# Optimization experiments

Measured on AMD Instinct MI355X. Metric: run time of the kernel, lower is better.

## Reference

```python
import jax, jax.numpy as jnp
import numpy as np

N_NODES = 2048   # active nodes fed to the GCN (= sum(state_flag==1))
N_EDGES = 4096
L = 4096         # obs_dim: padded node count after flag==0 insertions
NHID = 16
GCN_OUT = 16
H1 = 1024
DIN = L * (3 + GCN_OUT)  # 77824


def setup_inputs() -> dict:
    key = jax.random.key(0)
    ks = jax.random.split(key, 14)
    X = jax.random.normal(ks[0], (N_NODES, 1), dtype=jnp.float32)
    Z = jax.random.normal(ks[1], (N_EDGES, 1), dtype=jnp.float32)
    adj_e = jax.random.uniform(ks[2], (N_EDGES, N_EDGES), dtype=jnp.float32) / N_EDGES
    adj_v = jax.random.uniform(ks[3], (N_NODES, N_NODES), dtype=jnp.float32) / N_NODES
    T = jax.random.uniform(ks[4], (N_NODES, N_EDGES), dtype=jnp.float32) / N_EDGES
    state_cost = jax.random.normal(ks[5], (L,), dtype=jnp.float32)
    # exactly N_NODES ones -> static shapes for the vectorized insertion
    state_flag = (jnp.arange(L) % 2).astype(jnp.float32)
    state_dual = jax.random.uniform(ks[6], (N_NODES, 1), dtype=jnp.float32)
    # GCN params (CensNet-style node/edge GCN, eval mode -> no dropout)
    W1 = jax.random.normal(ks[7], (2, NHID), dtype=jnp.float32) * (1.0 / np.sqrt(2.0))
    b1 = jnp.zeros((NHID,), dtype=jnp.float32)
    W2 = jax.random.normal(ks[8], (NHID, GCN_OUT), dtype=jnp.float32) * (1.0 / np.sqrt(NHID))
    b2 = jnp.zeros((GCN_OUT,), dtype=jnp.float32)
    # v_net MLP params
    Wm1 = jax.random.normal(ks[9], (DIN, H1), dtype=jnp.float32) * (1.0 / np.sqrt(DIN))
    bm1 = jnp.zeros((H1,), dtype=jnp.float32)
    Wm2 = jax.random.normal(ks[10], (H1, H1), dtype=jnp.float32) * (1.0 / np.sqrt(H1))
    bm2 = jnp.zeros((H1,), dtype=jnp.float32)
    Wm3 = jax.random.normal(ks[11], (H1, 1), dtype=jnp.float32) * (1.0 / np.sqrt(H1))
    bm3 = jnp.zeros((1,), dtype=jnp.float32)
    return {"X": X, "Z": Z, "adj_e": adj_e, "adj_v": adj_v, "T": T,
            "state_cost": state_cost, "state_flag": state_flag, "state_dual": state_dual,
            "W1": W1, "b1": b1, "W2": W2, "b2": b2,
            "Wm1": Wm1, "bm1": bm1, "Wm2": Wm2, "bm2": bm2, "Wm3": Wm3, "bm3": bm3}


def reference(X, Z, adj_e, adj_v, T, state_cost, state_flag, state_dual,
              W1, b1, W2, b2, Wm1, bm1, Wm2, bm2, Wm3, bm3):
    # --- GCN(nfeat_v=1, nfeat_e=1) -> [N, GCN_OUT] node embeddings ---
    Ze = adj_e @ Z                                 # [E,1] edge convolution
    H0 = jnp.concatenate([X, T @ Ze], axis=1)      # [N,2] node feats + incidence-pooled edge feats
    Hh = jax.nn.relu(adj_v @ (H0 @ W1) + b1)       # [N, NHID]
    emb = adj_v @ (Hh @ W2) + b2                   # [N, GCN_OUT]

    # --- vectorized equivalent of the O(L^2) insertion loop ---
    # row i of the padded embedding is emb[rank_of_i_among_flag==1] if flag[i]==1 else 0
    flag_i = state_flag.astype(jnp.int32)
    src = jnp.clip(jnp.cumsum(flag_i) - 1, 0, emb.shape[0] - 1)   # [L]
    m = state_flag[:, None] > 0                                   # [L,1]
    emb_pad = jnp.where(m, emb[src], 0.0)                         # [L, GCN_OUT]
    dual_pad = jnp.where(m, state_dual[src], 1.0)                 # [L, 1]

    obs = jnp.concatenate([
        jax.nn.log_softmax(state_cost[:, None], axis=0),
        state_flag[:, None],
        dual_pad,
        emb_pad,
    ], axis=1).reshape(-1)                                        # [L*(3+GCN_OUT)]

    # --- v_net MLP: tanh, tanh, identity ---
    h = jnp.tanh(obs @ Wm1 + bm1)
    h = jnp.tanh(h @ Wm2 + bm2)
    v = h @ Wm3 + bm3                                             # [1]
    return jnp.squeeze(v, -1)                                     # scalar
```

## Files before the change

### kernel.cpp

```cpp
#include <hip/hip_runtime.h>
#include <math.h>

#define N_NODES 2048
#define N_EDGES 4096
#define L_DIM   4096
#define H1      1024
#define DIN     (L_DIM * 19)
#define NCHUNK1 1024
#define ROWS1   76
#define NCHUNK2 256
#define ROWS2   4

typedef float v4f __attribute__((ext_vector_type(4)));
__device__ __forceinline__ float4 ntload4(const float4* p) {
    v4f v = __builtin_nontemporal_load((const v4f*)p);
    float4 r; r.x = v.x; r.y = v.y; r.z = v.z; r.w = v.w;
    return r;
}

__global__ void gemv_rows(const float* __restrict__ A, const float* __restrict__ x,
                          float* __restrict__ y, int C4 ) {
    const int tid = threadIdx.x;
    const int row = blockIdx.x;
    const float4* A4 = (const float4*)A + (size_t)row * C4;
    const float4* X4 = (const float4*)x;
    float acc = 0.f;
    #pragma unroll 4
    for (int p = tid; p < C4; p += 256) {
        float4 a = ntload4(A4 + p);
        float4 b = X4[p];
        acc += a.x * b.x + a.y * b.y + a.z * b.z + a.w * b.w;
    }
    acc += __shfl_xor(acc, 1);  acc += __shfl_xor(acc, 2);  acc += __shfl_xor(acc, 4);
    acc += __shfl_xor(acc, 8);  acc += __shfl_xor(acc, 16); acc += __shfl_xor(acc, 32);
    __shared__ float s[4];
    if ((tid & 63) == 0) s[tid >> 6] = acc;
    __syncthreads();
    if (tid == 0) y[row] = s[0] + s[1] + s[2] + s[3];
}

__global__ void gemv_T_p1(const float* __restrict__ T, const float* __restrict__ Ze,
                          const float* __restrict__ X, const float* __restrict__ W1,
                          float* __restrict__ P1) {
    const int tid = threadIdx.x;
    const int row = blockIdx.x;
    const float4* A4 = (const float4*)T + (size_t)row * (N_EDGES / 4);
    const float4* X4 = (const float4*)Ze;
    float acc = 0.f;
    #pragma unroll 4
    for (int p = tid; p < N_EDGES / 4; p += 256) {
        float4 a = ntload4(A4 + p);
        float4 b = X4[p];
        acc += a.x * b.x + a.y * b.y + a.z * b.z + a.w * b.w;
    }
    acc += __shfl_xor(acc, 1);  acc += __shfl_xor(acc, 2);  acc += __shfl_xor(acc, 4);
    acc += __shfl_xor(acc, 8);  acc += __shfl_xor(acc, 16); acc += __shfl_xor(acc, 32);
    __shared__ float s[4];
    if ((tid & 63) == 0) s[tid >> 6] = acc;
    __syncthreads();
    if (tid < 16) {
        const float tze = s[0] + s[1] + s[2] + s[3];
        P1[(row >> 2) * 64 + tid * 4 + (row & 3)] = X[row] * W1[tid] + tze * W1[16 + tid];
    }
}

__global__ __launch_bounds__(256) void adjmul_lds(
        const float* __restrict__ A, const float* __restrict__ P,
        const float* __restrict__ bias, const float* __restrict__ W2,
        float* __restrict__ outp, int fuse_p2) {
    __shared__ float As[8][2052];
    __shared__ float hs[8][16];
    const int tid = threadIdx.x;
    const int row0 = blockIdx.x * 8;
    const float4* Ag = (const float4*)A;
    #pragma unroll
    for (int r = 0; r < 8; ++r) {
        float4 v0 = ntload4(Ag + (size_t)(row0 + r) * 512 + tid);
        float4 v1 = ntload4(Ag + (size_t)(row0 + r) * 512 + 256 + tid);
        *(float4*)&As[r][tid * 4] = v0;
        *(float4*)&As[r][1024 + tid * 4] = v1;
    }
    __syncthreads();

    const int row = tid >> 5, p = tid & 31;
    const float4* P4 = (const float4*)P;
    float acc[16];
    #pragma unroll
    for (int c = 0; c < 16; ++c) acc[c] = 0.f;
    #pragma unroll 2
    for (int it = 0; it < 16; ++it) {
        const int k4 = it * 32 + p;
        float4 a = *(const float4*)&As[row][k4 * 4];
        const float4* Pr = P4 + (size_t)k4 * 16;
        #pragma unroll
        for (int c = 0; c < 16; ++c) {
            float4 pv = Pr[c];
            acc[c] += a.x * pv.x + a.y * pv.y + a.z * pv.z + a.w * pv.w;
        }
    }
    #pragma unroll
    for (int c = 0; c < 16; ++c) {
        float v = acc[c];
        v += __shfl_xor(v, 1);  v += __shfl_xor(v, 2);  v += __shfl_xor(v, 4);
        v += __shfl_xor(v, 8);  v += __shfl_xor(v, 16);
        acc[c] = v;
    }

    if (fuse_p2) {
        if (p == 0) {
            #pragma unroll
            for (int c = 0; c < 16; ++c) hs[row][c] = fmaxf(acc[c] + bias[c], 0.f);
        }
        __syncthreads();
        if (tid < 128) {
            const int k = tid >> 4, c2 = tid & 15;
            float sv = 0.f;
            #pragma unroll
            for (int h = 0; h < 16; ++h) sv += hs[k][h] * W2[h * 16 + c2];
            const int kg = row0 + k;
            outp[(kg >> 2) * 64 + c2 * 4 + (kg & 3)] = sv;
        }
    } else {
        if (p == 0) {
            const int grow = row0 + row;
            #pragma unroll
            for (int c = 0; c < 16; ++c) outp[grow * 16 + c] = acc[c] + bias[c];
        }
    }
}

__global__ void prep_kernel(const float* __restrict__ flag, const float* __restrict__ cost,
                            int* __restrict__ src, float* __restrict__ lse) {
    __shared__ int   si[256];
    __shared__ float sf[256];
    const int tid = threadIdx.x;

    const int base = tid * 16;
    const float4* F4 = (const float4*)flag;
    float fv[16];
    #pragma unroll
    for (int q = 0; q < 4; ++q) {
        float4 v = F4[tid * 4 + q];
        fv[q * 4 + 0] = v.x; fv[q * 4 + 1] = v.y; fv[q * 4 + 2] = v.z; fv[q * 4 + 3] = v.w;
    }
    int f[16];
    int local = 0;
    #pragma unroll
    for (int e = 0; e < 16; ++e) {
        f[e] = fv[e] > 0.5f ? 1 : 0;
        local += f[e];
    }
    si[tid] = local;
    __syncthreads();
    #pragma unroll
    for (int off = 1; off < 256; off <<= 1) {
        int t = si[tid];
        if (tid >= off) t += si[tid - off];
        __syncthreads();
        si[tid] = t;
        __syncthreads();
    }
    int run = si[tid] - local;
    #pragma unroll
    for (int e = 0; e < 16; ++e) {
        run += f[e];
        int v = run - 1;
        v = v < 0 ? 0 : (v > N_NODES - 1 ? N_NODES - 1 : v);
        src[base + e] = v;
    }

    const float4* C4v = (const float4*)cost;
    float4 cv = C4v[tid * 4 + 0];
    float4 cw = C4v[tid * 4 + 1];
    float4 cy = C4v[tid * 4 + 2];
    float4 cz = C4v[tid * 4 + 3];
    float m = fmaxf(fmaxf(fmaxf(cv.x, cv.y), fmaxf(cv.z, cv.w)),
                    fmaxf(fmaxf(cw.x, cw.y), fmaxf(cw.z, cw.w)));
    m = fmaxf(m, fmaxf(fmaxf(fmaxf(cy.x, cy.y), fmaxf(cy.z, cy.w)),
                       fmaxf(fmaxf(cz.x, cz.y), fmaxf(cz.z, cz.w))));
    sf[tid] = m;
    __syncthreads();
    for (int off = 128; off > 0; off >>= 1) {
        if (tid < off) sf[tid] = fmaxf(sf[tid], sf[tid + off]);
        __syncthreads();
    }
    const float M = sf[0];
    __syncthreads();
    float sum = expf(cv.x - M) + expf(cv.y - M) + expf(cv.z - M) + expf(cv.w - M)
              + expf(cw.x - M) + expf(cw.y - M) + expf(cw.z - M) + expf(cw.w - M)
              + expf(cy.x - M) + expf(cy.y - M) + expf(cy.z - M) + expf(cy.w - M)
              + expf(cz.x - M) + expf(cz.y - M) + expf(cz.z - M) + expf(cz.w - M);
    sf[tid] = sum;
    __syncthreads();
    for (int off = 128; off > 0; off >>= 1) {
        if (tid < off) sf[tid] += sf[tid + off];
        __syncthreads();
    }
    if (tid == 0) lse[0] = M + logf(sf[0]);
}

__global__ void gemv_obs_wm1(const float* __restrict__ W, const float* __restrict__ cost,
                             const float* __restrict__ flag, const float* __restrict__ dual,
                             const float* __restrict__ emb, const int* __restrict__ src,
                             const float* __restrict__ lse, float* __restrict__ partial) {
    const int tid = threadIdx.x;
    const int row0 = blockIdx.x * ROWS1;
    __shared__ float xs[128];
    __shared__ float xv_c[128];
    __shared__ int   ri_c[128];
    __shared__ int   wcnt[2];
    __shared__ int   cnt_s;
    if (tid < ROWS1) {
        const int i_din = row0 + tid;
        const int i = i_din / 19;
        const int c = i_din - i * 19;
        const float fl = flag[i];
        float v;
        if (c == 0)      v = cost[i] - lse[0];
        else if (c == 1) v = fl;
        else if (c == 2) v = (fl > 0.5f) ? dual[src[i]] : 1.0f;
        else             v = (fl > 0.5f) ? emb[src[i] * 16 + (c - 3)] : 0.0f;
        xs[tid] = v;
    }
    __syncthreads();

    const bool pred = (tid < ROWS1) && (xs[tid] != 0.0f);
    const unsigned long long mask = __ballot(pred);
    const int lane = tid & 63, wid = tid >> 6;
    const int wpre = __popcll(mask & ((1ull << lane) - 1ull));
    if (lane == 0 && wid < 2) wcnt[wid] = __popcll(mask);
    __syncthreads();
    if (tid == 0) cnt_s = wcnt[0] + wcnt[1];
    __syncthreads();
    if (pred) {
        const int idx = (wid == 0 ? 0 : wcnt[0]) + wpre;
        xv_c[idx] = xs[tid];
        ri_c[idx] = tid;
    }
    __syncthreads();

    const int cnt = cnt_s;
    const float4* W4 = (const float4*)W;
    float4 acc = {0.f, 0.f, 0.f, 0.f};
    #pragma unroll 4
    for (int ii = 0; ii < cnt; ++ii) {
        const float xv = xv_c[ii];
        float4 w = ntload4(W4 + (size_t)(row0 + ri_c[ii]) * 256 + tid);
        acc.x += xv * w.x; acc.y += xv * w.y; acc.z += xv * w.z; acc.w += xv * w.w;
    }
    ((float4*)partial)[(size_t)blockIdx.x * 256 + tid] = acc;
}

__global__ void wm2_fused(const float* __restrict__ part1, const float* __restrict__ bm1,
                          const float* __restrict__ Wm2, float* __restrict__ part2) {
    const int tid = threadIdx.x;
    const int j0 = blockIdx.x * ROWS2;
    const int jj = tid & 3, kg = tid >> 2;
    float sum = 0.f;
    for (int k = kg; k < NCHUNK1; k += 64) sum += part1[(size_t)k * 1024 + j0 + jj];
    __shared__ float s[256];
    __shared__ float hsv[4];
    s[tid] = sum;
    __syncthreads();
    for (int off = 32; off > 0; off >>= 1) {
        if (kg < off) s[tid] += s[tid + off * 4];
        __syncthreads();
    }
    if (tid < 4) hsv[tid] = tanhf(s[tid] + bm1[j0 + tid]);
    __syncthreads();

    const float4* W4 = (const float4*)Wm2;
    float4 acc = {0.f, 0.f, 0.f, 0.f};
    #pragma unroll
    for (int i = 0; i < ROWS2; ++i) {
        const float xv = hsv[i];
        float4 w = ntload4(W4 + (size_t)(j0 + i) * 256 + tid);
        acc.x += xv * w.x; acc.y += xv * w.y; acc.z += xv * w.z; acc.w += xv * w.w;
    }
    ((float4*)part2)[(size_t)blockIdx.x * 256 + tid] = acc;
}

__global__ void reduce_cols(const float* __restrict__ partial, int nchunk,
                            const float* __restrict__ bias, float* __restrict__ out,
                            int do_tanh) {
    const int tid = threadIdx.x;
    const int jj = tid & 63, kg = tid >> 6;
    const int j = blockIdx.x * 64 + jj;
    float sum = 0.f;
    for (int k = kg; k < nchunk; k += 4) sum += partial[(size_t)k * 1024 + j];
    __shared__ float s[256];
    s[tid] = sum;
    __syncthreads();
    if (kg < 2) s[tid] += s[tid + 128];
    __syncthreads();
    if (kg == 0) {
        float v = s[tid] + s[tid + 64] + bias[j];
        out[j] = do_tanh ? tanhf(v) : v;
    }
}

__global__ void final_dot(const float* __restrict__ h, const float* __restrict__ w,
                          const float* __restrict__ b, float* __restrict__ out) {
    const int tid = threadIdx.x;
    float4 a  = ((const float4*)h)[tid];
    float4 ww = ((const float4*)w)[tid];
    float acc = a.x * ww.x + a.y * ww.y + a.z * ww.z + a.w * ww.w;
    __shared__ float s[256];
    s[tid] = acc;
    __syncthreads();
    for (int off = 128; off > 0; off >>= 1) {
        if (tid < off) s[tid] += s[tid + off];
        __syncthreads();
    }
    if (tid == 0) out[0] = s[0] + b[0];
}

extern "C" void kernel_launch(void* const* d_in, const int* in_sizes, int n_in,
                              void* d_out, int out_size, void* d_ws, size_t ws_size,
                              hipStream_t stream) {
    const float* X      = (const float*)d_in[0];
    const float* Z      = (const float*)d_in[1];
    const float* adj_e  = (const float*)d_in[2];
    const float* adj_v  = (const float*)d_in[3];
    const float* T      = (const float*)d_in[4];
    const float* cost   = (const float*)d_in[5];
    const float* flag   = (const float*)d_in[6];
    const float* dual   = (const float*)d_in[7];
    const float* W1     = (const float*)d_in[8];
    const float* b1     = (const float*)d_in[9];
    const float* W2     = (const float*)d_in[10];
    const float* b2     = (const float*)d_in[11];
    const float* Wm1    = (const float*)d_in[12];
    const float* bm1    = (const float*)d_in[13];
    const float* Wm2    = (const float*)d_in[14];
    const float* bm2    = (const float*)d_in[15];
    const float* Wm3    = (const float*)d_in[16];
    const float* bm3    = (const float*)d_in[17];
    float* out = (float*)d_out;

    char* ws = (char*)d_ws;
    float* Ze    = (float*)(ws + 0);
    float* P1    = (float*)(ws + 16384);
    float* P2    = (float*)(ws + 147456);
    float* emb   = (float*)(ws + 278528);
    int*   src   = (int*)  (ws + 409600);
    float* lse   = (float*)(ws + 425984);
    float* part1 = (float*)(ws + 426240);
    float* part2 = (float*)(ws + 4620544);
    float* h2    = (float*)(ws + 5669120);

    prep_kernel<<<1, 256, 0, stream>>>(flag, cost, src, lse);

    gemv_rows<<<N_EDGES, 256, 0, stream>>>(adj_e, Z, Ze, N_EDGES / 4);
    gemv_T_p1<<<N_NODES, 256, 0, stream>>>(T, Ze, X, W1, P1);
    adjmul_lds<<<N_NODES / 8, 256, 0, stream>>>(adj_v, P1, b1, W2, P2, 1);
    adjmul_lds<<<N_NODES / 8, 256, 0, stream>>>(adj_v, P2, b2, W2, emb, 0);

    gemv_obs_wm1<<<NCHUNK1, 256, 0, stream>>>(Wm1, cost, flag, dual, emb,
                                              src, lse, part1);
    wm2_fused<<<NCHUNK2, 256, 0, stream>>>(part1, bm1, Wm2, part2);
    reduce_cols<<<16, 256, 0, stream>>>(part2, NCHUNK2, bm2, h2, 1);
    final_dot<<<1, 256, 0, stream>>>(h2, Wm3, bm3, out);
}
```

Before: 568.2 us.

## Fuse whole pipeline into one cooperative persistent kernel with grid syncs

Replaces the nine separate launches with one cooperative kernel of 1024 blocks that runs every stage in turn (adj_e GEMV, T GEMV, two adj_v multiplies, the sparse-skipping Wm1 GEMV, Wm2, reduction, final dot), separated by grid.sync. The goal is to remove launch gaps and tail effects between the many small stages. The adj_v stages now read straight from global memory instead of staging rows in LDS, and each block handles fewer rows. It falls back to the old multi-kernel path if the cooperative launch fails, and grid-wide barriers add their own synchronisation cost.

```diff
diff --git a/kernel.cpp b/kernel.cpp
--- a/kernel.cpp
+++ b/kernel.cpp
@@ -1,12 +1,13 @@
 #include <hip/hip_runtime.h>
+#include <hip/hip_cooperative_groups.h>
 #include <math.h>
+
+namespace cg = cooperative_groups;
 
 #define N_NODES 2048
 #define N_EDGES 4096
 #define L_DIM   4096
-#define H1      1024
-#define DIN     (L_DIM * 19)
-#define NCHUNK1 1024
+#define NBLK    1024
 #define ROWS1   76
 #define NCHUNK2 256
 #define ROWS2   4
@@ -17,22 +18,324 @@
     float4 r; r.x = v.x; r.y = v.y; r.z = v.z; r.w = v.w;
     return r;
 }
+__device__ __forceinline__ float dot4(float4 a, float4 b) {
+    return a.x * b.x + a.y * b.y + a.z * b.z + a.w * b.w;
+}
+__device__ __forceinline__ float wred(float v) {
+    v += __shfl_xor(v, 1);  v += __shfl_xor(v, 2);  v += __shfl_xor(v, 4);
+    v += __shfl_xor(v, 8);  v += __shfl_xor(v, 16); v += __shfl_xor(v, 32);
+    return v;
+}
+
+struct KP {
+    const float *X, *Z, *adj_e, *adj_v, *T, *cost, *flag, *dual;
+    const float *W1, *b1, *W2, *b2, *Wm1, *bm1, *Wm2, *bm2, *Wm3, *bm3;
+    float *out;
+    float *Ze, *P1, *P2, *emb; int *src; float *lse;
+    float *part1, *part2, *h2;
+};
+
+__global__ __launch_bounds__(256, 4) void fused_all(KP P) {
+    cg::grid_group grid = cg::this_grid();
+    const int tid  = threadIdx.x;
+    const int bid  = blockIdx.x;
+    const int lane = tid & 63, wid = tid >> 6;
+
+    __shared__ float sred[4][4];
+    __shared__ float stze[2];
+    __shared__ int   si[256];
+    __shared__ float scratch[256];
+    __shared__ float wsl[4][16];
+    __shared__ float hsC[2][16];
+    __shared__ float hsvF[4];
+    __shared__ float xsE[128];
+    __shared__ float xvE[128];
+    __shared__ int   riE[128];
+    __shared__ int   wcE[2];
+    __shared__ int   cntE;
+
+    {
+        const int r0 = bid * 4;
+        const float4* Z4 = (const float4*)P.Z;
+        const float4* A0 = (const float4*)P.adj_e + (size_t)r0 * 1024;
+        float a0 = 0.f, a1 = 0.f, a2 = 0.f, a3 = 0.f;
+        #pragma unroll
+        for (int q = 0; q < 4; ++q) {
+            const int p = tid + q * 256;
+            float4 zv = Z4[p];
+            a0 += dot4(ntload4(A0 + p), zv);
+            a1 += dot4(ntload4(A0 + 1024 + p), zv);
+            a2 += dot4(ntload4(A0 + 2048 + p), zv);
+            a3 += dot4(ntload4(A0 + 3072 + p), zv);
+        }
+        a0 = wred(a0); a1 = wred(a1); a2 = wred(a2); a3 = wred(a3);
+        if (lane == 0) { sred[wid][0] = a0; sred[wid][1] = a1;
+                         sred[wid][2] = a2; sred[wid][3] = a3; }
+        __syncthreads();
+        if (tid < 4)
+            P.Ze[r0 + tid] = sred[0][tid] + sred[1][tid] + sred[2][tid] + sred[3][tid];
+
+        if (bid == 0) {
+            const int base = tid * 16;
+            const float4* F4 = (const float4*)P.flag;
+            float fv[16];
+            #pragma unroll
+            for (int q = 0; q < 4; ++q) {
+                float4 v = F4[tid * 4 + q];
+                fv[q*4+0] = v.x; fv[q*4+1] = v.y; fv[q*4+2] = v.z; fv[q*4+3] = v.w;
+            }
+            int f[16]; int local = 0;
+            #pragma unroll
+            for (int e = 0; e < 16; ++e) { f[e] = fv[e] > 0.5f ? 1 : 0; local += f[e]; }
+            si[tid] = local;
+            __syncthreads();
+            #pragma unroll
+            for (int off = 1; off < 256; off <<= 1) {
+                int t = si[tid];
+                if (tid >= off) t += si[tid - off];
+                __syncthreads();
+                si[tid] = t;
+                __syncthreads();
+            }
+            int run = si[tid] - local;
+            #pragma unroll
+            for (int e = 0; e < 16; ++e) {
+                run += f[e];
+                int v = run - 1;
+                v = v < 0 ? 0 : (v > N_NODES - 1 ? N_NODES - 1 : v);
+                P.src[base + e] = v;
+            }
+            const float4* C4v = (const float4*)P.cost;
+            float4 cv = C4v[tid*4+0], cw = C4v[tid*4+1];
+            float4 cy = C4v[tid*4+2], cz = C4v[tid*4+3];
+            float m = fmaxf(fmaxf(fmaxf(cv.x,cv.y), fmaxf(cv.z,cv.w)),
+                            fmaxf(fmaxf(cw.x,cw.y), fmaxf(cw.z,cw.w)));
+            m = fmaxf(m, fmaxf(fmaxf(fmaxf(cy.x,cy.y), fmaxf(cy.z,cy.w)),
+                               fmaxf(fmaxf(cz.x,cz.y), fmaxf(cz.z,cz.w))));
+            scratch[tid] = m;
+            __syncthreads();
+            for (int off = 128; off > 0; off >>= 1) {
+                if (tid < off) scratch[tid] = fmaxf(scratch[tid], scratch[tid + off]);
+                __syncthreads();
+            }
+            const float M = scratch[0];
+            __syncthreads();
+            float sum = expf(cv.x-M)+expf(cv.y-M)+expf(cv.z-M)+expf(cv.w-M)
+                      + expf(cw.x-M)+expf(cw.y-M)+expf(cw.z-M)+expf(cw.w-M)
+                      + expf(cy.x-M)+expf(cy.y-M)+expf(cy.z-M)+expf(cy.w-M)
+                      + expf(cz.x-M)+expf(cz.y-M)+expf(cz.z-M)+expf(cz.w-M);
+            scratch[tid] = sum;
+            __syncthreads();
+            for (int off = 128; off > 0; off >>= 1) {
+                if (tid < off) scratch[tid] += scratch[tid + off];
+                __syncthreads();
+            }
+            if (tid == 0) P.lse[0] = M + logf(scratch[0]);
+        }
+    }
+    grid.sync();
+
+    const int rB = bid * 2;
+    {
+        const float4* Ze4 = (const float4*)P.Ze;
+        const float4* T0  = (const float4*)P.T + (size_t)rB * 1024;
+        float a0 = 0.f, a1 = 0.f;
+        #pragma unroll
+        for (int q = 0; q < 4; ++q) {
+            const int p = tid + q * 256;
+            float4 zv = Ze4[p];
+            a0 += dot4(ntload4(T0 + p), zv);
+            a1 += dot4(ntload4(T0 + 1024 + p), zv);
+        }
+        a0 = wred(a0); a1 = wred(a1);
+        if (lane == 0) { sred[wid][0] = a0; sred[wid][1] = a1; }
+        __syncthreads();
+        if (tid < 2) stze[tid] = sred[0][tid] + sred[1][tid] + sred[2][tid] + sred[3][tid];
+        __syncthreads();
+        if (tid < 32) {
+            const int rr = tid >> 4, c = tid & 15;
+            const int row = rB + rr;
+            P.P1[(row >> 2) * 64 + c * 4 + (row & 3)] =
+                P.X[row] * P.W1[c] + stze[rr] * P.W1[16 + c];
+        }
+    }
+    grid.sync();
+
+    {
+        const int row = tid >> 7, p = tid & 127;
+        const int r = rB + row;
+        const float4* Av  = (const float4*)P.adj_v + (size_t)r * 512;
+        const float4* P1v = (const float4*)P.P1;
+        float acc[16];
+        #pragma unroll
+        for (int c = 0; c < 16; ++c) acc[c] = 0.f;
+        #pragma unroll
+        for (int it = 0; it < 4; ++it) {
+            const int k4 = it * 128 + p;
+            float4 a = ntload4(Av + k4);
+            const float4* Pr = P1v + (size_t)k4 * 16;
+            #pragma unroll
+            for (int c = 0; c < 16; ++c) {
+                float4 pv = Pr[c];
+                acc[c] += dot4(a, pv);
+            }
+        }
+        #pragma unroll
+        for (int c = 0; c < 16; ++c) {
+            float v = wred(acc[c]);
+            if (lane == 0) wsl[wid][c] = v;
+        }
+        __syncthreads();
+        if (tid < 32) {
+            const int rr = tid >> 4, c = tid & 15;
+            hsC[rr][c] = fmaxf(wsl[2*rr][c] + wsl[2*rr+1][c] + P.b1[c], 0.f);
+        }
+        __syncthreads();
+        if (tid < 32) {
+            const int rr = tid >> 4, c2 = tid & 15;
+            float sv = 0.f;
+            #pragma unroll
+            for (int h = 0; h < 16; ++h) sv += hsC[rr][h] * P.W2[h * 16 + c2];
+            const int k = rB + rr;
+            P.P2[(k >> 2) * 64 + c2 * 4 + (k & 3)] = sv;
+        }
+    }
+    grid.sync();
+
+    {
+        const int row = tid >> 7, p = tid & 127;
+        const int r = rB + row;
+        const float4* Av  = (const float4*)P.adj_v + (size_t)r * 512;
+        const float4* P2v = (const float4*)P.P2;
+        float acc[16];
+        #pragma unroll
+        for (int c = 0; c < 16; ++c) acc[c] = 0.f;
+        #pragma unroll
+        for (int it = 0; it < 4; ++it) {
+            const int k4 = it * 128 + p;
+            float4 a = ntload4(Av + k4);
+            const float4* Pr = P2v + (size_t)k4 * 16;
+            #pragma unroll
+            for (int c = 0; c < 16; ++c) {
+                float4 pv = Pr[c];
+                acc[c] += dot4(a, pv);
+            }
+        }
+        #pragma unroll
+        for (int c = 0; c < 16; ++c) {
+            float v = wred(acc[c]);
+            if (lane == 0) wsl[wid][c] = v;
+        }
+        __syncthreads();
+        if (tid < 32) {
+            const int rr = tid >> 4, c = tid & 15;
+            P.emb[(rB + rr) * 16 + c] = wsl[2*rr][c] + wsl[2*rr+1][c] + P.b2[c];
+        }
+    }
+    grid.sync();
+
+    {
+        const int row0 = bid * ROWS1;
+        if (tid < ROWS1) {
+            const int i_din = row0 + tid;
+            const int i = i_din / 19;
+            const int c = i_din - i * 19;
+            const float fl = P.flag[i];
+            float v;
+            if (c == 0)      v = P.cost[i] - P.lse[0];
+            else if (c == 1) v = fl;
+            else if (c == 2) v = (fl > 0.5f) ? P.dual[P.src[i]] : 1.0f;
+            else             v = (fl > 0.5f) ? P.emb[P.src[i] * 16 + (c - 3)] : 0.0f;
+            xsE[tid] = v;
+        }
+        __syncthreads();
+        const bool pred = (tid < ROWS1) && (xsE[tid] != 0.0f);
+        const unsigned long long mask = __ballot(pred);
+        const int wpre = __popcll(mask & ((1ull << lane) - 1ull));
+        if (lane == 0 && wid < 2) wcE[wid] = __popcll(mask);
+        __syncthreads();
+        if (tid == 0) cntE = wcE[0] + wcE[1];
+        __syncthreads();
+        if (pred) {
+            const int idx = (wid == 0 ? 0 : wcE[0]) + wpre;
+            xvE[idx] = xsE[tid];
+            riE[idx] = tid;
+        }
+        __syncthreads();
+        const int cnt = cntE;
+        const float4* W4 = (const float4*)P.Wm1;
+        float4 acc = {0.f, 0.f, 0.f, 0.f};
+        #pragma unroll 4
+        for (int ii = 0; ii < cnt; ++ii) {
+            const float xv = xvE[ii];
+            float4 w = ntload4(W4 + (size_t)(row0 + riE[ii]) * 256 + tid);
+            acc.x += xv*w.x; acc.y += xv*w.y; acc.z += xv*w.z; acc.w += xv*w.w;
+        }
+        ((float4*)P.part1)[(size_t)bid * 256 + tid] = acc;
+    }
+    grid.sync();
+
+    if (bid < 256) {
+        const int j0 = bid * 4;
+        const int jj = tid & 3, kg = tid >> 2;
+        float sum = 0.f;
+        for (int k = kg; k < NBLK; k += 64) sum += P.part1[(size_t)k * 1024 + j0 + jj];
+        scratch[tid] = sum;
+        __syncthreads();
+        for (int off = 32; off > 0; off >>= 1) {
+            if (kg < off) scratch[tid] += scratch[tid + off * 4];
+            __syncthreads();
+        }
+        if (tid < 4) hsvF[tid] = tanhf(scratch[tid] + P.bm1[j0 + tid]);
+        __syncthreads();
+        const float4* W4 = (const float4*)P.Wm2;
+        float4 acc = {0.f, 0.f, 0.f, 0.f};
+        #pragma unroll
+        for (int i = 0; i < 4; ++i) {
+            const float xv = hsvF[i];
+            float4 w = ntload4(W4 + (size_t)(j0 + i) * 256 + tid);
+            acc.x += xv*w.x; acc.y += xv*w.y; acc.z += xv*w.z; acc.w += xv*w.w;
+        }
+        ((float4*)P.part2)[(size_t)bid * 256 + tid] = acc;
+    }
+    grid.sync();
+
+    if (bid < 16) {
+        const int jj = tid & 63, kg = tid >> 6;
+        const int j = bid * 64 + jj;
+        float sum = 0.f;
+        for (int k = kg; k < 256; k += 4) sum += P.part2[(size_t)k * 1024 + j];
+        scratch[tid] = sum;
+        __syncthreads();
+        if (kg < 2) scratch[tid] += scratch[tid + 128];
+        __syncthreads();
+        if (kg == 0) P.h2[j] = tanhf(scratch[tid] + scratch[tid + 64] + P.bm2[j]);
+    }
+    grid.sync();
+
+    if (bid == 0) {
+        float4 a  = ((const float4*)P.h2)[tid];
+        float4 ww = ((const float4*)P.Wm3)[tid];
+        scratch[tid] = dot4(a, ww);
+        __syncthreads();
+        for (int off = 128; off > 0; off >>= 1) {
+            if (tid < off) scratch[tid] += scratch[tid + off];
+            __syncthreads();
+        }
+        if (tid == 0) P.out[0] = scratch[0] + P.bm3[0];
+    }
+}
 
 __global__ void gemv_rows(const float* __restrict__ A, const float* __restrict__ x,
-                          float* __restrict__ y, int C4 ) {
+                          float* __restrict__ y, int C4) {
     const int tid = threadIdx.x;
     const int row = blockIdx.x;
     const float4* A4 = (const float4*)A + (size_t)row * C4;
     const float4* X4 = (const float4*)x;
     float acc = 0.f;
     #pragma unroll 4
-    for (int p = tid; p < C4; p += 256) {
-        float4 a = ntload4(A4 + p);
-        float4 b = X4[p];
-        acc += a.x * b.x + a.y * b.y + a.z * b.z + a.w * b.w;
-    }
-    acc += __shfl_xor(acc, 1);  acc += __shfl_xor(acc, 2);  acc += __shfl_xor(acc, 4);
-    acc += __shfl_xor(acc, 8);  acc += __shfl_xor(acc, 16); acc += __shfl_xor(acc, 32);
+    for (int p = tid; p < C4; p += 256) acc += dot4(ntload4(A4 + p), X4[p]);
+    acc = wred(acc);
     __shared__ float s[4];
     if ((tid & 63) == 0) s[tid >> 6] = acc;
     __syncthreads();
@@ -48,13 +351,8 @@
     const float4* X4 = (const float4*)Ze;
     float acc = 0.f;
     #pragma unroll 4
-    for (int p = tid; p < N_EDGES / 4; p += 256) {
-        float4 a = ntload4(A4 + p);
-        float4 b = X4[p];
-        acc += a.x * b.x + a.y * b.y + a.z * b.z + a.w * b.w;
-    }
-    acc += __shfl_xor(acc, 1);  acc += __shfl_xor(acc, 2);  acc += __shfl_xor(acc, 4);
-    acc += __shfl_xor(acc, 8);  acc += __shfl_xor(acc, 16); acc += __shfl_xor(acc, 32);
+    for (int p = tid; p < N_EDGES / 4; p += 256) acc += dot4(ntload4(A4 + p), X4[p]);
+    acc = wred(acc);
     __shared__ float s[4];
     if ((tid & 63) == 0) s[tid >> 6] = acc;
     __syncthreads();
@@ -81,7 +379,6 @@
         *(float4*)&As[r][1024 + tid * 4] = v1;
     }
     __syncthreads();
-
     const int row = tid >> 5, p = tid & 31;
     const float4* P4 = (const float4*)P;
     float acc[16];
@@ -93,10 +390,7 @@
         float4 a = *(const float4*)&As[row][k4 * 4];
         const float4* Pr = P4 + (size_t)k4 * 16;
         #pragma unroll
-        for (int c = 0; c < 16; ++c) {
-            float4 pv = Pr[c];
-            acc[c] += a.x * pv.x + a.y * pv.y + a.z * pv.z + a.w * pv.w;
-        }
+        for (int c = 0; c < 16; ++c) acc[c] += dot4(a, Pr[c]);
     }
     #pragma unroll
     for (int c = 0; c < 16; ++c) {
@@ -105,7 +399,6 @@
         v += __shfl_xor(v, 8);  v += __shfl_xor(v, 16);
         acc[c] = v;
     }
-
     if (fuse_p2) {
         if (p == 0) {
             #pragma unroll
@@ -134,22 +427,17 @@
     __shared__ int   si[256];
     __shared__ float sf[256];
     const int tid = threadIdx.x;
-
     const int base = tid * 16;
     const float4* F4 = (const float4*)flag;
     float fv[16];
     #pragma unroll
     for (int q = 0; q < 4; ++q) {
         float4 v = F4[tid * 4 + q];
-        fv[q * 4 + 0] = v.x; fv[q * 4 + 1] = v.y; fv[q * 4 + 2] = v.z; fv[q * 4 + 3] = v.w;
-    }
-    int f[16];
-    int local = 0;
-    #pragma unroll
-    for (int e = 0; e < 16; ++e) {
-        f[e] = fv[e] > 0.5f ? 1 : 0;
-        local += f[e];
-    }
+        fv[q*4+0] = v.x; fv[q*4+1] = v.y; fv[q*4+2] = v.z; fv[q*4+3] = v.w;
+    }
+    int f[16]; int local = 0;
+    #pragma unroll
+    for (int e = 0; e < 16; ++e) { f[e] = fv[e] > 0.5f ? 1 : 0; local += f[e]; }
     si[tid] = local;
     __syncthreads();
     #pragma unroll
@@ -168,16 +456,13 @@
         v = v < 0 ? 0 : (v > N_NODES - 1 ? N_NODES - 1 : v);
         src[base + e] = v;
     }
-
     const float4* C4v = (const float4*)cost;
-    float4 cv = C4v[tid * 4 + 0];
-    float4 cw = C4v[tid * 4 + 1];
-    float4 cy = C4v[tid * 4 + 2];
-    float4 cz = C4v[tid * 4 + 3];
-    float m = fmaxf(fmaxf(fmaxf(cv.x, cv.y), fmaxf(cv.z, cv.w)),
-                    fmaxf(fmaxf(cw.x, cw.y), fmaxf(cw.z, cw.w)));
-    m = fmaxf(m, fmaxf(fmaxf(fmaxf(cy.x, cy.y), fmaxf(cy.z, cy.w)),
-                       fmaxf(fmaxf(cz.x, cz.y), fmaxf(cz.z, cz.w))));
+    float4 cv = C4v[tid*4+0], cw = C4v[tid*4+1];
+    float4 cy = C4v[tid*4+2], cz = C4v[tid*4+3];
+    float m = fmaxf(fmaxf(fmaxf(cv.x,cv.y), fmaxf(cv.z,cv.w)),
+                    fmaxf(fmaxf(cw.x,cw.y), fmaxf(cw.z,cw.w)));
+    m = fmaxf(m, fmaxf(fmaxf(fmaxf(cy.x,cy.y), fmaxf(cy.z,cy.w)),
+                       fmaxf(fmaxf(cz.x,cz.y), fmaxf(cz.z,cz.w))));
     sf[tid] = m;
     __syncthreads();
     for (int off = 128; off > 0; off >>= 1) {
@@ -186,10 +471,10 @@
     }
     const float M = sf[0];
     __syncthreads();
-    float sum = expf(cv.x - M) + expf(cv.y - M) + expf(cv.z - M) + expf(cv.w - M)
-              + expf(cw.x - M) + expf(cw.y - M) + expf(cw.z - M) + expf(cw.w - M)
-              + expf(cy.x - M) + expf(cy.y - M) + expf(cy.z - M) + expf(cy.w - M)
-              + expf(cz.x - M) + expf(cz.y - M) + expf(cz.z - M) + expf(cz.w - M);
+    float sum = expf(cv.x-M)+expf(cv.y-M)+expf(cv.z-M)+expf(cv.w-M)
+              + expf(cw.x-M)+expf(cw.y-M)+expf(cw.z-M)+expf(cw.w-M)
+              + expf(cy.x-M)+expf(cy.y-M)+expf(cy.z-M)+expf(cy.w-M)
+              + expf(cz.x-M)+expf(cz.y-M)+expf(cz.z-M)+expf(cz.w-M);
     sf[tid] = sum;
     __syncthreads();
     for (int off = 128; off > 0; off >>= 1) {
@@ -223,7 +508,6 @@
         xs[tid] = v;
     }
     __syncthreads();
-
     const bool pred = (tid < ROWS1) && (xs[tid] != 0.0f);
     const unsigned long long mask = __ballot(pred);
     const int lane = tid & 63, wid = tid >> 6;
@@ -238,7 +522,6 @@
         ri_c[idx] = tid;
     }
     __syncthreads();
-
     const int cnt = cnt_s;
     const float4* W4 = (const float4*)W;
     float4 acc = {0.f, 0.f, 0.f, 0.f};
@@ -246,7 +529,7 @@
     for (int ii = 0; ii < cnt; ++ii) {
         const float xv = xv_c[ii];
         float4 w = ntload4(W4 + (size_t)(row0 + ri_c[ii]) * 256 + tid);
-        acc.x += xv * w.x; acc.y += xv * w.y; acc.z += xv * w.z; acc.w += xv * w.w;
+        acc.x += xv*w.x; acc.y += xv*w.y; acc.z += xv*w.z; acc.w += xv*w.w;
     }
     ((float4*)partial)[(size_t)blockIdx.x * 256 + tid] = acc;
 }
@@ -257,7 +540,7 @@
     const int j0 = blockIdx.x * ROWS2;
     const int jj = tid & 3, kg = tid >> 2;
     float sum = 0.f;
-    for (int k = kg; k < NCHUNK1; k += 64) sum += part1[(size_t)k * 1024 + j0 + jj];
+    for (int k = kg; k < NBLK; k += 64) sum += part1[(size_t)k * 1024 + j0 + jj];
     __shared__ float s[256];
     __shared__ float hsv[4];
     s[tid] = sum;
@@ -268,14 +551,13 @@
     }
     if (tid < 4) hsv[tid] = tanhf(s[tid] + bm1[j0 + tid]);
     __syncthreads();
-
     const float4* W4 = (const float4*)Wm2;
     float4 acc = {0.f, 0.f, 0.f, 0.f};
     #pragma unroll
     for (int i = 0; i < ROWS2; ++i) {
         const float xv = hsv[i];
         float4 w = ntload4(W4 + (size_t)(j0 + i) * 256 + tid);
-        acc.x += xv * w.x; acc.y += xv * w.y; acc.z += xv * w.z; acc.w += xv * w.w;
+        acc.x += xv*w.x; acc.y += xv*w.y; acc.z += xv*w.z; acc.w += xv*w.w;
     }
     ((float4*)part2)[(size_t)blockIdx.x * 256 + tid] = acc;
 }
@@ -304,7 +586,7 @@
     const int tid = threadIdx.x;
     float4 a  = ((const float4*)h)[tid];
     float4 ww = ((const float4*)w)[tid];
-    float acc = a.x * ww.x + a.y * ww.y + a.z * ww.z + a.w * ww.w;
+    float acc = dot4(a, ww);
     __shared__ float s[256];
     s[tid] = acc;
     __syncthreads();
@@ -318,47 +600,50 @@
 extern "C" void kernel_launch(void* const* d_in, const int* in_sizes, int n_in,
                               void* d_out, int out_size, void* d_ws, size_t ws_size,
                               hipStream_t stream) {
-    const float* X      = (const float*)d_in[0];
-    const float* Z      = (const float*)d_in[1];
-    const float* adj_e  = (const float*)d_in[2];
-    const float* adj_v  = (const float*)d_in[3];
-    const float* T      = (const float*)d_in[4];
-    const float* cost   = (const float*)d_in[5];
-    const float* flag   = (const float*)d_in[6];
-    const float* dual   = (const float*)d_in[7];
-    const float* W1     = (const float*)d_in[8];
-    const float* b1     = (const float*)d_in[9];
-    const float* W2     = (const float*)d_in[10];
-    const float* b2     = (const float*)d_in[11];
-    const float* Wm1    = (const float*)d_in[12];
-    const float* bm1    = (const float*)d_in[13];
-    const float* Wm2    = (const float*)d_in[14];
-    const float* bm2    = (const float*)d_in[15];
-    const float* Wm3    = (const float*)d_in[16];
-    const float* bm3    = (const float*)d_in[17];
-    float* out = (float*)d_out;
-
     char* ws = (char*)d_ws;
-    float* Ze    = (float*)(ws + 0);
-    float* P1    = (float*)(ws + 16384);
-    float* P2    = (float*)(ws + 147456);
-    float* emb   = (float*)(ws + 278528);
-    int*   src   = (int*)  (ws + 409600);
-    float* lse   = (float*)(ws + 425984);
-    float* part1 = (float*)(ws + 426240);
-    float* part2 = (float*)(ws + 4620544);
-    float* h2    = (float*)(ws + 5669120);
-
-    prep_kernel<<<1, 256, 0, stream>>>(flag, cost, src, lse);
-
-    gemv_rows<<<N_EDGES, 256, 0, stream>>>(adj_e, Z, Ze, N_EDGES / 4);
-    gemv_T_p1<<<N_NODES, 256, 0, stream>>>(T, Ze, X, W1, P1);
-    adjmul_lds<<<N_NODES / 8, 256, 0, stream>>>(adj_v, P1, b1, W2, P2, 1);
-    adjmul_lds<<<N_NODES / 8, 256, 0, stream>>>(adj_v, P2, b2, W2, emb, 0);
-
-    gemv_obs_wm1<<<NCHUNK1, 256, 0, stream>>>(Wm1, cost, flag, dual, emb,
-                                              src, lse, part1);
-    wm2_fused<<<NCHUNK2, 256, 0, stream>>>(part1, bm1, Wm2, part2);
-    reduce_cols<<<16, 256, 0, stream>>>(part2, NCHUNK2, bm2, h2, 1);
-    final_dot<<<1, 256, 0, stream>>>(h2, Wm3, bm3, out);
-}
+    KP kp;
+    kp.X     = (const float*)d_in[0];
+    kp.Z     = (const float*)d_in[1];
+    kp.adj_e = (const float*)d_in[2];
+    kp.adj_v = (const float*)d_in[3];
+    kp.T     = (const float*)d_in[4];
+    kp.cost  = (const float*)d_in[5];
+    kp.flag  = (const float*)d_in[6];
+    kp.dual  = (const float*)d_in[7];
+    kp.W1    = (const float*)d_in[8];
+    kp.b1    = (const float*)d_in[9];
+    kp.W2    = (const float*)d_in[10];
+    kp.b2    = (const float*)d_in[11];
+    kp.Wm1   = (const float*)d_in[12];
+    kp.bm1   = (const float*)d_in[13];
+    kp.Wm2   = (const float*)d_in[14];
+    kp.bm2   = (const float*)d_in[15];
+    kp.Wm3   = (const float*)d_in[16];
+    kp.bm3   = (const float*)d_in[17];
+    kp.out   = (float*)d_out;
+    kp.Ze    = (float*)(ws + 0);
+    kp.P1    = (float*)(ws + 16384);
+    kp.P2    = (float*)(ws + 147456);
+    kp.emb   = (float*)(ws + 278528);
+    kp.src   = (int*)  (ws + 409600);
+    kp.lse   = (float*)(ws + 425984);
+    kp.part1 = (float*)(ws + 426240);
+    kp.part2 = (float*)(ws + 4620544);
+    kp.h2    = (float*)(ws + 5669120);
+
+    void* kargs[] = { (void*)&kp };
+    hipError_t err = hipLaunchCooperativeKernel(reinterpret_cast<void*>(&fused_all),
+                                                dim3(NBLK), dim3(256), kargs, 0, stream);
+    if (err != hipSuccess) {
+        prep_kernel<<<1, 256, 0, stream>>>(kp.flag, kp.cost, kp.src, kp.lse);
+        gemv_rows<<<N_EDGES, 256, 0, stream>>>(kp.adj_e, kp.Z, kp.Ze, N_EDGES / 4);
+        gemv_T_p1<<<N_NODES, 256, 0, stream>>>(kp.T, kp.Ze, kp.X, kp.W1, kp.P1);
+        adjmul_lds<<<N_NODES / 8, 256, 0, stream>>>(kp.adj_v, kp.P1, kp.b1, kp.W2, kp.P2, 1);
+        adjmul_lds<<<N_NODES / 8, 256, 0, stream>>>(kp.adj_v, kp.P2, kp.b2, kp.W2, kp.emb, 0);
+        gemv_obs_wm1<<<NBLK, 256, 0, stream>>>(kp.Wm1, kp.cost, kp.flag, kp.dual,
+                                               kp.emb, kp.src, kp.lse, kp.part1);
+        wm2_fused<<<NCHUNK2, 256, 0, stream>>>(kp.part1, kp.bm1, kp.Wm2, kp.part2);
+        reduce_cols<<<16, 256, 0, stream>>>(kp.part2, NCHUNK2, kp.bm2, kp.h2, 1);
+        final_dot<<<1, 256, 0, stream>>>(kp.h2, kp.Wm3, kp.bm3, kp.out);
+    }
+}
```

Result: slower. 1.483 ms (+161.0%).
